# Optimization experiments

Measured on AMD Instinct MI355X. Metric: run time of the kernel, lower is better.

The kernel has to match this reference:

```python
import jax, jax.numpy as jnp
import numpy as np


def setup_inputs() -> dict:
    key = jax.random.key(0)
    ks = jax.random.split(key, 6)
    B, C, H, W = 2, 256, 128, 512
    img1 = jax.random.normal(ks[0], (B, C, H, W), jnp.float32)
    img2 = jax.random.normal(ks[1], (B, C, H, W), jnp.float32)
    intri1 = jax.random.uniform(ks[2], (B, 3, 3), jnp.float32)
    intri2 = jax.random.uniform(ks[3], (B, 3, 3), jnp.float32)
    extri1 = jax.random.uniform(ks[4], (B, 4, 4), jnp.float32)
    extri2 = jax.random.uniform(ks[5], (B, 4, 4), jnp.float32)
    return {"img1": img1, "img2": img2, "intri1": intri1, "intri2": intri2,
            "extri1": extri1, "extri2": extri2}


TEMPERATURE = 1.0  # init default
DISP_CLAMP = 0.1   # from corresp_prob_to_depth_conf


def reference(img1, img2, intri1, intri2, extri1, extri2):
    """CostVolume(dot, dual=False, pack_lr=False, geometry_mask=True).forward.
    Returns (depth, confidence), each (B, 1, H, W). G=1 group dim kept.
    """
    B, C, H, W = img1.shape
    # full per-row correlation volume: vol[b,h,w1,w2] = <img1[:,w1], img2[:,w2]> / sqrt(C)
    vol = jnp.einsum('bchw,bchv->bhwv', img1, img2) / jnp.asarray(np.sqrt(C), img1.dtype)
    idx = jnp.arange(W, dtype=vol.dtype)
    # left_first=True -> lower-triangular geometry mask (correspondence w2 <= w1)
    tril = (idx[None, :] <= idx[:, None]).astype(vol.dtype)  # (W1, W2)
    # NOTE: mask is applied AFTER softmax (prob is NOT renormalized), as in source
    prob = jax.nn.softmax(vol / TEMPERATURE, axis=-1) * tril  # (B,H,W1,W2)
    corresp = jnp.sum(prob * idx, axis=-1)[:, None]  # soft-argmax index, (B,1,H,W)
    confidence = jnp.max(prob, axis=-1)[:, None]      # (B,1,H,W)
    # corresp2disp with normalize=True (normalized_intri default True)
    disp = jnp.abs(corresp - idx) / W
    disp = jnp.clip(disp, DISP_CLAMP)
    # d2d_transform (reconstructed): pinhole disparity->depth, depth = fx * baseline / disp
    fx = intri1[:, 0, 0][:, None, None, None]
    baseline = jnp.linalg.norm(extri1[:, :3, 3] - extri2[:, :3, 3], axis=-1)[:, None, None, None]
    depth = fx * baseline / disp
    return depth, confidence
```

## Files before the change

kernel.cpp:

```cpp
#include <hip/hip_runtime.h>

typedef __attribute__((ext_vector_type(4))) float f32x4;
typedef __attribute__((ext_vector_type(8))) short s16x8;

#define C_DIM 256
#define H_DIM 128
#define W_DIM 512
#define HW    (H_DIM * W_DIM)
#define CHW   (C_DIM * HW)

__device__ __forceinline__ unsigned short f2bf(float f) {
    unsigned u = __builtin_bit_cast(unsigned, f);
    u = (u + 0x7FFFu + ((u >> 16) & 1u)) >> 16;
    return (unsigned short)u;
}

__global__ __launch_bounds__(512, 4) void costvol_kernel(
    const float* __restrict__ img1, const float* __restrict__ img2,
    const float* __restrict__ intri1,
    const float* __restrict__ extri1, const float* __restrict__ extri2,
    float* __restrict__ out)
{
    __shared__ __align__(16) unsigned char smem[32768];
    unsigned short* Alds = (unsigned short*)smem;

    const int t = threadIdx.x;
    const int d = blockIdx.x;
    const int win = d >> 6, pos = d & 63;
    const int bh    = win * 8 + (pos & 7);
    const int w1blk = pos >> 3;
    const int b = bh >> 7, h = bh & 127;
    const int w1base = w1blk * 64;

    const float* i1 = img1 + (size_t)b * CHW + (size_t)h * W_DIM;
    const float* i2 = img2 + (size_t)b * CHW + (size_t)h * W_DIM;

    {
        const int c    = t >> 1;
        const int wseg = (t & 1) << 5;
        const float* src = i1 + (size_t)c * HW + (size_t)(w1base + wseg);
        #pragma unroll
        for (int i0 = 0; i0 < 32; i0 += 4) {
            f32x4 v = *(const f32x4*)(src + i0);
            #pragma unroll
            for (int j = 0; j < 4; ++j) {
                const int w = wseg + i0 + j;
                Alds[w * 256 + ((((c >> 3) ^ (w & 15)) << 3) | (c & 7))] = f2bf(v[j]);
            }
        }
    }
    __syncthreads();

    const int wn = t >> 6, lane = t & 63;
    const int lrow = lane & 15, hq = lane >> 4;

    const float* pb[4];
    #pragma unroll
    for (int ct = 0; ct < 4; ++ct)
        pb[ct] = i2 + (size_t)(8 * hq) * HW + (64 * wn + 16 * ct + lrow);

    f32x4 acc[4][4] = {};

    for (int kc = 0; kc < 8; ++kc) {
        s16x8 afr[4];
        #pragma unroll
        for (int rt = 0; rt < 4; ++rt) {
            const int row = 16 * rt + lrow;
            const int kb  = (kc << 2) + hq;
            afr[rt] = *(const s16x8*)&Alds[row * 256 + ((kb ^ (row & 15)) << 3)];
        }
        #pragma unroll
        for (int ct = 0; ct < 4; ++ct) {
            const float* p = pb[ct] + (size_t)(32 * kc) * HW;
            float f[8];
            #pragma unroll
            for (int j = 0; j < 8; ++j) f[j] = p[(size_t)j * HW];
            unsigned dw[4];
            #pragma unroll
            for (int q = 0; q < 4; ++q)
                dw[q] = (unsigned)f2bf(f[2 * q]) | ((unsigned)f2bf(f[2 * q + 1]) << 16);
            s16x8 bfr;
            #pragma unroll
            for (int q = 0; q < 4; ++q) {
                bfr[2 * q]     = (short)(dw[q] & 0xFFFFu);
                bfr[2 * q + 1] = (short)(dw[q] >> 16);
            }
            #pragma unroll
            for (int rt = 0; rt < 4; ++rt)
                acc[rt][ct] = __builtin_amdgcn_mfma_f32_16x16x32_bf16(afr[rt], bfr, acc[rt][ct], 0, 0, 0);
        }
    }

    __syncthreads();

    float (*red)[64][3] = (float(*)[64][3])smem;
    #pragma unroll
    for (int rt = 0; rt < 4; ++rt) {
        #pragma unroll
        for (int r = 0; r < 4; ++r) {
            const int row = 16 * rt + 4 * hq + r;
            const int w1g = w1base + row;
            float Se = 0.f, Sei = 0.f, Me = 0.f;
            #pragma unroll
            for (int ct = 0; ct < 4; ++ct) {
                const int col = 64 * wn + 16 * ct + lrow;
                const float e = __expf(acc[rt][ct][r] * 0.0625f);
                Se += e;
                if (col <= w1g) { Sei += e * (float)col; Me = fmaxf(Me, e); }
            }
            #pragma unroll
            for (int m = 1; m < 16; m <<= 1) {
                Se  += __shfl_xor(Se,  m, 64);
                Sei += __shfl_xor(Sei, m, 64);
                Me   = fmaxf(Me, __shfl_xor(Me, m, 64));
            }
            if (lrow == 0) {
                red[wn][row][0] = Se;
                red[wn][row][1] = Sei;
                red[wn][row][2] = Me;
            }
        }
    }
    __syncthreads();

    if (t < 64) {
        const int row = t;
        float Se = 0.f, Sei = 0.f, Me = 0.f;
        #pragma unroll
        for (int q = 0; q < 8; ++q) {
            Se  += red[q][row][0];
            Sei += red[q][row][1];
            Me   = fmaxf(Me, red[q][row][2]);
        }
        const int w1g = w1base + row;
        const float corresp = Sei / Se;
        const float conf    = Me / Se;
        float disp = fabsf(corresp - (float)w1g) * (1.0f / 512.0f);
        disp = fmaxf(disp, 0.1f);
        const float fx = intri1[b * 9];
        const float dx = extri1[b * 16 + 3]  - extri2[b * 16 + 3];
        const float dy = extri1[b * 16 + 7]  - extri2[b * 16 + 7];
        const float dz = extri1[b * 16 + 11] - extri2[b * 16 + 11];
        const float bl = sqrtf(dx * dx + dy * dy + dz * dz);
        const float depth = fx * bl / disp;
        const int oidx = b * HW + h * W_DIM + w1g;
        out[oidx]          = depth;
        out[2 * HW + oidx] = conf;
    }
}

extern "C" void kernel_launch(void* const* d_in, const int* in_sizes, int n_in,
                              void* d_out, int out_size, void* d_ws, size_t ws_size,
                              hipStream_t stream) {
    const float* img1   = (const float*)d_in[0];
    const float* img2   = (const float*)d_in[1];
    const float* intri1 = (const float*)d_in[2];
    const float* extri1 = (const float*)d_in[4];
    const float* extri2 = (const float*)d_in[5];
    costvol_kernel<<<dim3(2048), dim3(512), 0, stream>>>(
        img1, img2, intri1, extri1, extri2, (float*)d_out);
}
```

Before: 127.7 us.

## Pre-transpose img2 to bf16 channel-contiguous workspace before cost-volume GEMM

```diff
diff --git a/kernel.cpp b/kernel.cpp
--- a/kernel.cpp
+++ b/kernel.cpp
@@ -8,6 +8,7 @@
 #define W_DIM 512
 #define HW    (H_DIM * W_DIM)
 #define CHW   (C_DIM * HW)
+#define WS_NEED (2ull * 128 * 512 * 256 * 2)
 
 __device__ __forceinline__ unsigned short f2bf(float f) {
     unsigned u = __builtin_bit_cast(unsigned, f);
@@ -15,8 +16,40 @@
     return (unsigned short)u;
 }
 
+__global__ __launch_bounds__(256) void transpose_kernel(
+    const float* __restrict__ img2, unsigned short* __restrict__ bws)
+{
+    __shared__ unsigned short tile[64][65];
+    const int t = threadIdx.x;
+    const int d = blockIdx.x;
+    const int cb = d & 3, wb = (d >> 2) & 7, bh = d >> 5;
+    const float* src = img2 + (size_t)bh * W_DIM + (size_t)(cb * 64) * HW + wb * 64;
+
+    {
+        const int c = t >> 2, w0 = (t & 3) << 4;
+        const float* p = src + (size_t)c * HW + w0;
+        #pragma unroll
+        for (int i = 0; i < 16; i += 4) {
+            f32x4 v = *(const f32x4*)(p + i);
+            #pragma unroll
+            for (int j = 0; j < 4; ++j) tile[c][w0 + i + j] = f2bf(v[j]);
+        }
+    }
+    __syncthreads();
+
+    {
+        const int n_l = t >> 2, c4 = (t & 3) << 4;
+        unsigned short vals[16];
+        #pragma unroll
+        for (int i = 0; i < 16; ++i) vals[i] = tile[c4 + i][n_l];
+        unsigned short* dst = bws + ((size_t)bh * 512 + wb * 64 + n_l) * 256 + cb * 64 + c4;
+        *(s16x8*)(dst)     = *(s16x8*)&vals[0];
+        *(s16x8*)(dst + 8) = *(s16x8*)&vals[8];
+    }
+}
+
 __global__ __launch_bounds__(512, 4) void costvol_kernel(
-    const float* __restrict__ img1, const float* __restrict__ img2,
+    const float* __restrict__ img1, const unsigned short* __restrict__ bws,
     const float* __restrict__ intri1,
     const float* __restrict__ extri1, const float* __restrict__ extri2,
     float* __restrict__ out)
@@ -33,7 +66,6 @@
     const int w1base = w1blk * 64;
 
     const float* i1 = img1 + (size_t)b * CHW + (size_t)h * W_DIM;
-    const float* i2 = img2 + (size_t)b * CHW + (size_t)h * W_DIM;
 
     {
         const int c    = t >> 1;
@@ -54,13 +86,14 @@
     const int wn = t >> 6, lane = t & 63;
     const int lrow = lane & 15, hq = lane >> 4;
 
-    const float* pb[4];
+    const unsigned short* pb[4];
     #pragma unroll
     for (int ct = 0; ct < 4; ++ct)
-        pb[ct] = i2 + (size_t)(8 * hq) * HW + (64 * wn + 16 * ct + lrow);
+        pb[ct] = bws + ((size_t)bh * 512 + 64 * wn + 16 * ct + lrow) * 256 + 8 * hq;
 
     f32x4 acc[4][4] = {};
 
+    #pragma unroll
     for (int kc = 0; kc < 8; ++kc) {
         s16x8 afr[4];
         #pragma unroll
@@ -71,20 +104,7 @@
         }
         #pragma unroll
         for (int ct = 0; ct < 4; ++ct) {
-            const float* p = pb[ct] + (size_t)(32 * kc) * HW;
-            float f[8];
-            #pragma unroll
-            for (int j = 0; j < 8; ++j) f[j] = p[(size_t)j * HW];
-            unsigned dw[4];
-            #pragma unroll
-            for (int q = 0; q < 4; ++q)
-                dw[q] = (unsigned)f2bf(f[2 * q]) | ((unsigned)f2bf(f[2 * q + 1]) << 16);
-            s16x8 bfr;
-            #pragma unroll
-            for (int q = 0; q < 4; ++q) {
-                bfr[2 * q]     = (short)(dw[q] & 0xFFFFu);
-                bfr[2 * q + 1] = (short)(dw[q] >> 16);
-            }
+            const s16x8 bfr = *(const s16x8*)(pb[ct] + (kc << 5));
             #pragma unroll
             for (int rt = 0; rt < 4; ++rt)
                 acc[rt][ct] = __builtin_amdgcn_mfma_f32_16x16x32_bf16(afr[rt], bfr, acc[rt][ct], 0, 0, 0);
@@ -149,6 +169,116 @@
     }
 }
 
+__global__ __launch_bounds__(512, 4) void costvol_fallback(
+    const float* __restrict__ img1, const float* __restrict__ img2,
+    const float* __restrict__ intri1,
+    const float* __restrict__ extri1, const float* __restrict__ extri2,
+    float* __restrict__ out)
+{
+    __shared__ __align__(16) unsigned char smem[32768];
+    unsigned short* Alds = (unsigned short*)smem;
+    const int t = threadIdx.x;
+    const int d = blockIdx.x;
+    const int win = d >> 6, pos = d & 63;
+    const int bh    = win * 8 + (pos & 7);
+    const int w1blk = pos >> 3;
+    const int b = bh >> 7, h = bh & 127;
+    const int w1base = w1blk * 64;
+    const float* i1 = img1 + (size_t)b * CHW + (size_t)h * W_DIM;
+    const float* i2 = img2 + (size_t)b * CHW + (size_t)h * W_DIM;
+    {
+        const int c    = t >> 1;
+        const int wseg = (t & 1) << 5;
+        const float* src = i1 + (size_t)c * HW + (size_t)(w1base + wseg);
+        #pragma unroll
+        for (int i0 = 0; i0 < 32; i0 += 4) {
+            f32x4 v = *(const f32x4*)(src + i0);
+            #pragma unroll
+            for (int j = 0; j < 4; ++j) {
+                const int w = wseg + i0 + j;
+                Alds[w * 256 + ((((c >> 3) ^ (w & 15)) << 3) | (c & 7))] = f2bf(v[j]);
+            }
+        }
+    }
+    __syncthreads();
+    const int wn = t >> 6, lane = t & 63;
+    const int lrow = lane & 15, hq = lane >> 4;
+    const float* pb[4];
+    #pragma unroll
+    for (int ct = 0; ct < 4; ++ct)
+        pb[ct] = i2 + (size_t)(8 * hq) * HW + (64 * wn + 16 * ct + lrow);
+    f32x4 acc[4][4] = {};
+    for (int kc = 0; kc < 8; ++kc) {
+        s16x8 afr[4];
+        #pragma unroll
+        for (int rt = 0; rt < 4; ++rt) {
+            const int row = 16 * rt + lrow;
+            const int kb  = (kc << 2) + hq;
+            afr[rt] = *(const s16x8*)&Alds[row * 256 + ((kb ^ (row & 15)) << 3)];
+        }
+        #pragma unroll
+        for (int ct = 0; ct < 4; ++ct) {
+            const float* p = pb[ct] + (size_t)(32 * kc) * HW;
+            float f[8];
+            #pragma unroll
+            for (int j = 0; j < 8; ++j) f[j] = p[(size_t)j * HW];
+            s16x8 bfr;
+            #pragma unroll
+            for (int j = 0; j < 8; ++j) bfr[j] = (short)f2bf(f[j]);
+            #pragma unroll
+            for (int rt = 0; rt < 4; ++rt)
+                acc[rt][ct] = __builtin_amdgcn_mfma_f32_16x16x32_bf16(afr[rt], bfr, acc[rt][ct], 0, 0, 0);
+        }
+    }
+    __syncthreads();
+    float (*red)[64][3] = (float(*)[64][3])smem;
+    #pragma unroll
+    for (int rt = 0; rt < 4; ++rt) {
+        #pragma unroll
+        for (int r = 0; r < 4; ++r) {
+            const int row = 16 * rt + 4 * hq + r;
+            const int w1g = w1base + row;
+            float Se = 0.f, Sei = 0.f, Me = 0.f;
+            #pragma unroll
+            for (int ct = 0; ct < 4; ++ct) {
+                const int col = 64 * wn + 16 * ct + lrow;
+                const float e = __expf(acc[rt][ct][r] * 0.0625f);
+                Se += e;
+                if (col <= w1g) { Sei += e * (float)col; Me = fmaxf(Me, e); }
+            }
+            #pragma unroll
+            for (int m = 1; m < 16; m <<= 1) {
+                Se  += __shfl_xor(Se,  m, 64);
+                Sei += __shfl_xor(Sei, m, 64);
+                Me   = fmaxf(Me, __shfl_xor(Me, m, 64));
+            }
+            if (lrow == 0) { red[wn][row][0] = Se; red[wn][row][1] = Sei; red[wn][row][2] = Me; }
+        }
+    }
+    __syncthreads();
+    if (t < 64) {
+        const int row = t;
+        float Se = 0.f, Sei = 0.f, Me = 0.f;
+        #pragma unroll
+        for (int q = 0; q < 8; ++q) {
+            Se += red[q][row][0]; Sei += red[q][row][1]; Me = fmaxf(Me, red[q][row][2]);
+        }
+        const int w1g = w1base + row;
+        const float corresp = Sei / Se;
+        const float conf    = Me / Se;
+        float disp = fabsf(corresp - (float)w1g) * (1.0f / 512.0f);
+        disp = fmaxf(disp, 0.1f);
+        const float fx = intri1[b * 9];
+        const float dx = extri1[b * 16 + 3]  - extri2[b * 16 + 3];
+        const float dy = extri1[b * 16 + 7]  - extri2[b * 16 + 7];
+        const float dz = extri1[b * 16 + 11] - extri2[b * 16 + 11];
+        const float bl = sqrtf(dx * dx + dy * dy + dz * dz);
+        const int oidx = b * HW + h * W_DIM + w1g;
+        out[oidx]          = fx * bl / disp;
+        out[2 * HW + oidx] = conf;
+    }
+}
+
 extern "C" void kernel_launch(void* const* d_in, const int* in_sizes, int n_in,
                               void* d_out, int out_size, void* d_ws, size_t ws_size,
                               hipStream_t stream) {
@@ -157,6 +287,13 @@
     const float* intri1 = (const float*)d_in[2];
     const float* extri1 = (const float*)d_in[4];
     const float* extri2 = (const float*)d_in[5];
-    costvol_kernel<<<dim3(2048), dim3(512), 0, stream>>>(
-        img1, img2, intri1, extri1, extri2, (float*)d_out);
-}
+    if (ws_size >= WS_NEED) {
+        unsigned short* bws = (unsigned short*)d_ws;
+        transpose_kernel<<<dim3(8192), dim3(256), 0, stream>>>(img2, bws);
+        costvol_kernel<<<dim3(2048), dim3(512), 0, stream>>>(
+            img1, bws, intri1, extri1, extri2, (float*)d_out);
+    } else {
+        costvol_fallback<<<dim3(2048), dim3(512), 0, stream>>>(
+            img1, img2, intri1, extri1, extri2, (float*)d_out);
+    }
+}
```

New measurement: 158.0 us. +23.7%, slower.

## Halve w1 tile per block, transpose MFMA operands, prescale A by 1/sqrt(C)

Applied to the files above, without the earlier changes.

```diff
diff --git a/kernel.cpp b/kernel.cpp
--- a/kernel.cpp
+++ b/kernel.cpp
@@ -1,4 +1,5 @@
 #include <hip/hip_runtime.h>
+#include <hip/hip_bf16.h>
 
 typedef __attribute__((ext_vector_type(4))) float f32x4;
 typedef __attribute__((ext_vector_type(8))) short s16x8;
@@ -10,9 +11,7 @@
 #define CHW   (C_DIM * HW)
 
 __device__ __forceinline__ unsigned short f2bf(float f) {
-    unsigned u = __builtin_bit_cast(unsigned, f);
-    u = (u + 0x7FFFu + ((u >> 16) & 1u)) >> 16;
-    return (unsigned short)u;
+    return __builtin_bit_cast(unsigned short, __float2bfloat16(f));
 }
 
 __global__ __launch_bounds__(512, 4) void costvol_kernel(
@@ -21,31 +20,31 @@
     const float* __restrict__ extri1, const float* __restrict__ extri2,
     float* __restrict__ out)
 {
-    __shared__ __align__(16) unsigned char smem[32768];
+    __shared__ __align__(16) unsigned char smem[16384];
     unsigned short* Alds = (unsigned short*)smem;
 
     const int t = threadIdx.x;
     const int d = blockIdx.x;
-    const int win = d >> 6, pos = d & 63;
-    const int bh    = win * 8 + (pos & 7);
+    const int pos = d & 127;
+    const int bh    = (d >> 7) * 8 + (pos & 7);
     const int w1blk = pos >> 3;
     const int b = bh >> 7, h = bh & 127;
-    const int w1base = w1blk * 64;
+    const int w1base = w1blk * 32;
 
     const float* i1 = img1 + (size_t)b * CHW + (size_t)h * W_DIM;
     const float* i2 = img2 + (size_t)b * CHW + (size_t)h * W_DIM;
 
     {
-        const int c    = t >> 1;
-        const int wseg = (t & 1) << 5;
-        const float* src = i1 + (size_t)c * HW + (size_t)(w1base + wseg);
+        const int c  = t >> 1;
+        const int w0 = (t & 1) << 4;
+        const float* src = i1 + (size_t)c * HW + (size_t)(w1base + w0);
         #pragma unroll
-        for (int i0 = 0; i0 < 32; i0 += 4) {
+        for (int i0 = 0; i0 < 16; i0 += 4) {
             f32x4 v = *(const f32x4*)(src + i0);
             #pragma unroll
             for (int j = 0; j < 4; ++j) {
-                const int w = wseg + i0 + j;
-                Alds[w * 256 + ((((c >> 3) ^ (w & 15)) << 3) | (c & 7))] = f2bf(v[j]);
+                const int w = w0 + i0 + j;
+                Alds[w * 256 + ((((c >> 3) ^ (w & 15)) << 3) | (c & 7))] = f2bf(v[j] * 0.0625f);
             }
         }
     }
@@ -56,74 +55,65 @@
 
     const float* pb[4];
     #pragma unroll
-    for (int ct = 0; ct < 4; ++ct)
-        pb[ct] = i2 + (size_t)(8 * hq) * HW + (64 * wn + 16 * ct + lrow);
+    for (int w2t = 0; w2t < 4; ++w2t)
+        pb[w2t] = i2 + (size_t)(8 * hq) * HW + (64 * wn + 16 * w2t + lrow);
 
-    f32x4 acc[4][4] = {};
+    f32x4 acc[4][2] = {};
 
     for (int kc = 0; kc < 8; ++kc) {
-        s16x8 afr[4];
+        s16x8 afr[2];
         #pragma unroll
-        for (int rt = 0; rt < 4; ++rt) {
-            const int row = 16 * rt + lrow;
+        for (int w1t = 0; w1t < 2; ++w1t) {
+            const int row = 16 * w1t + lrow;
             const int kb  = (kc << 2) + hq;
-            afr[rt] = *(const s16x8*)&Alds[row * 256 + ((kb ^ (row & 15)) << 3)];
+            afr[w1t] = *(const s16x8*)&Alds[row * 256 + ((kb ^ (row & 15)) << 3)];
         }
         #pragma unroll
-        for (int ct = 0; ct < 4; ++ct) {
-            const float* p = pb[ct] + (size_t)(32 * kc) * HW;
+        for (int w2t = 0; w2t < 4; ++w2t) {
+            const float* p = pb[w2t] + (size_t)(32 * kc) * HW;
             float f[8];
             #pragma unroll
             for (int j = 0; j < 8; ++j) f[j] = p[(size_t)j * HW];
-            unsigned dw[4];
-            #pragma unroll
-            for (int q = 0; q < 4; ++q)
-                dw[q] = (unsigned)f2bf(f[2 * q]) | ((unsigned)f2bf(f[2 * q + 1]) << 16);
             s16x8 bfr;
             #pragma unroll
-            for (int q = 0; q < 4; ++q) {
-                bfr[2 * q]     = (short)(dw[q] & 0xFFFFu);
-                bfr[2 * q + 1] = (short)(dw[q] >> 16);
-            }
+            for (int j = 0; j < 8; ++j) bfr[j] = (short)f2bf(f[j]);
             #pragma unroll
-            for (int rt = 0; rt < 4; ++rt)
-                acc[rt][ct] = __builtin_amdgcn_mfma_f32_16x16x32_bf16(afr[rt], bfr, acc[rt][ct], 0, 0, 0);
+            for (int w1t = 0; w1t < 2; ++w1t)
+                acc[w2t][w1t] = __builtin_amdgcn_mfma_f32_16x16x32_bf16(
+                    bfr, afr[w1t], acc[w2t][w1t], 0, 0, 0);
         }
     }
 
     __syncthreads();
 
-    float (*red)[64][3] = (float(*)[64][3])smem;
+    float (*red)[32][3] = (float(*)[32][3])smem;
     #pragma unroll
-    for (int rt = 0; rt < 4; ++rt) {
+    for (int w1t = 0; w1t < 2; ++w1t) {
+        const int w1l = 16 * w1t + lrow;
+        const int w1g = w1base + w1l;
+        float Se = 0.f, Sei = 0.f, Me = 0.f;
         #pragma unroll
-        for (int r = 0; r < 4; ++r) {
-            const int row = 16 * rt + 4 * hq + r;
-            const int w1g = w1base + row;
-            float Se = 0.f, Sei = 0.f, Me = 0.f;
+        for (int w2t = 0; w2t < 4; ++w2t) {
             #pragma unroll
-            for (int ct = 0; ct < 4; ++ct) {
-                const int col = 64 * wn + 16 * ct + lrow;
-                const float e = __expf(acc[rt][ct][r] * 0.0625f);
+            for (int r = 0; r < 4; ++r) {
+                const int w2 = 64 * wn + 16 * w2t + 4 * hq + r;
+                const float e = __expf(acc[w2t][w1t][r]);
                 Se += e;
-                if (col <= w1g) { Sei += e * (float)col; Me = fmaxf(Me, e); }
+                if (w2 <= w1g) { Sei += e * (float)w2; Me = fmaxf(Me, e); }
             }
-            #pragma unroll
-            for (int m = 1; m < 16; m <<= 1) {
-                Se  += __shfl_xor(Se,  m, 64);
-                Sei += __shfl_xor(Sei, m, 64);
-                Me   = fmaxf(Me, __shfl_xor(Me, m, 64));
-            }
-            if (lrow == 0) {
-                red[wn][row][0] = Se;
-                red[wn][row][1] = Sei;
-                red[wn][row][2] = Me;
-            }
+        }
+        Se  += __shfl_xor(Se, 16, 64);  Se  += __shfl_xor(Se, 32, 64);
+        Sei += __shfl_xor(Sei, 16, 64); Sei += __shfl_xor(Sei, 32, 64);
+        Me = fmaxf(Me, __shfl_xor(Me, 16, 64)); Me = fmaxf(Me, __shfl_xor(Me, 32, 64));
+        if (hq == 0) {
+            red[wn][w1l][0] = Se;
+            red[wn][w1l][1] = Sei;
+            red[wn][w1l][2] = Me;
         }
     }
     __syncthreads();
 
-    if (t < 64) {
+    if (t < 32) {
         const int row = t;
         float Se = 0.f, Sei = 0.f, Me = 0.f;
         #pragma unroll
@@ -157,6 +147,6 @@
     const float* intri1 = (const float*)d_in[2];
     const float* extri1 = (const float*)d_in[4];
     const float* extri2 = (const float*)d_in[5];
-    costvol_kernel<<<dim3(2048), dim3(512), 0, stream>>>(
+    costvol_kernel<<<dim3(4096), dim3(512), 0, stream>>>(
         img1, img2, intri1, extri1, extri2, (float*)d_out);
 }
```

Result: slower. 162.2 us (+27.0%).
